# Kernel tuning notes

Measured on AMD Instinct MI355X. Metric: run time of the kernel, lower is better.

## Reference

```python
import jax, jax.numpy as jnp
import numpy as np

B, S, DIM, HEADS, DHEAD = 1, 1992, 2048, 16, 128
NKI_SEQ_ALIGN = 128
EPS = 1e-6


def setup_inputs() -> dict:
    key = jax.random.key(0)
    ks = jax.random.split(key, 8)
    hidden_states = jax.random.normal(ks[0], (B, S, DIM), dtype=jnp.float32)
    # realistic rotary tables, full head_dim with interleaved pair angles
    pos = jnp.arange(S, dtype=jnp.float32)
    inv_freq = 1.0 / (10000.0 ** (jnp.arange(0, DHEAD, 2, dtype=jnp.float32) / DHEAD))
    ang = pos[:, None] * inv_freq[None, :]                      # [S, DHEAD/2]
    full = jnp.stack([ang, ang], axis=-1).reshape(S, DHEAD)     # interleave
    freqs_cos = jnp.cos(full)[None, :, None, :]                 # [1,S,1,DHEAD]
    freqs_sin = jnp.sin(full)[None, :, None, :]
    sc = 0.02
    wq = jax.random.normal(ks[1], (DIM, DIM), dtype=jnp.float32) * sc
    wk = jax.random.normal(ks[2], (DIM, DIM), dtype=jnp.float32) * sc
    wv = jax.random.normal(ks[3], (DIM, DIM), dtype=jnp.float32) * sc
    wo = jax.random.normal(ks[4], (DIM, DIM), dtype=jnp.float32) * sc
    bq = jax.random.normal(ks[5], (DIM,), dtype=jnp.float32) * sc
    bk = jax.random.normal(ks[6], (DIM,), dtype=jnp.float32) * sc
    bv = jax.random.normal(ks[7], (DIM,), dtype=jnp.float32) * sc
    bo = jnp.zeros((DIM,), dtype=jnp.float32)
    norm_q_w = jnp.ones((DIM,), dtype=jnp.float32)
    norm_k_w = jnp.ones((DIM,), dtype=jnp.float32)
    return dict(hidden_states=hidden_states, freqs_cos=freqs_cos, freqs_sin=freqs_sin,
                wq=wq, bq=bq, wk=wk, bk=bk, wv=wv, bv=bv,
                norm_q_w=norm_q_w, norm_k_w=norm_k_w, wo=wo, bo=bo)


def _rms_norm(x, weight, eps=EPS):
    xf = x.astype(jnp.float32)
    var = jnp.mean(xf * xf, axis=-1, keepdims=True)
    return (weight * (xf * jax.lax.rsqrt(var + eps))).astype(x.dtype)


def _apply_rope(x, freqs_cos, freqs_sin):
    # x: [B,H,S,D]; freqs: [1,S,1,D]
    cos = jnp.transpose(freqs_cos[..., 0::2], (0, 2, 1, 3))  # [1,1,S,D/2]
    sin = jnp.transpose(freqs_sin[..., 1::2], (0, 2, 1, 3))
    x1, x2 = x[..., 0::2], x[..., 1::2]
    o1 = x1 * cos - x2 * sin
    o2 = x1 * sin + x2 * cos
    return jnp.stack([o1, o2], axis=-1).reshape(x.shape)


def _attention_padded(q, k, v):
    # Faithful to nki_flash_attention: zero-pad seq to multiple of 128,
    # no masking of padded keys (they contribute logit 0), trim query pad.
    B_, H_, S_, D_ = q.shape
    pad = (-S_) % NKI_SEQ_ALIGN
    if pad:
        pc = [(0, 0), (0, 0), (0, pad), (0, 0)]
        q = jnp.pad(q, pc); k = jnp.pad(k, pc); v = jnp.pad(v, pc)
    scale = 1.0 / np.sqrt(D_)
    scores = jnp.einsum('bhqd,bhkd->bhqk', q, k) * scale
    probs = jax.nn.softmax(scores, axis=-1)
    out = jnp.einsum('bhqk,bhkd->bhqd', probs, v)
    return out[:, :, :S_, :]


def reference(hidden_states, freqs_cos, freqs_sin, wq, bq, wk, bk, wv, bv,
              norm_q_w, norm_k_w, wo, bo):
    b, s, _ = hidden_states.shape
    q = hidden_states @ wq.T + bq
    k = hidden_states @ wk.T + bk
    v = hidden_states @ wv.T + bv
    q = _rms_norm(q, norm_q_w)
    k = _rms_norm(k, norm_k_w)
    hd = q.shape[-1] // HEADS
    q = q.reshape(b, s, HEADS, hd).transpose(0, 2, 1, 3)
    k = k.reshape(b, s, HEADS, hd).transpose(0, 2, 1, 3)
    v = v.reshape(b, s, HEADS, hd).transpose(0, 2, 1, 3)
    q = _apply_rope(q, freqs_cos, freqs_sin)
    k = _apply_rope(k, freqs_cos, freqs_sin)
    o = _attention_padded(q, k, v)
    o = o.transpose(0, 2, 1, 3).reshape(b, s, -1)
    return o @ wo.T + bo
```

## Files before the change

kernel.cpp:

```cpp
#include <hip/hip_runtime.h>
#include <cstdint>

#define S_REAL 1992
#define S_PAD  2048
#define DIMSZ  2048
#define NHEAD  16
#define DHD    128

typedef float f32x4 __attribute__((ext_vector_type(4)));
typedef float f32x16 __attribute__((ext_vector_type(16)));
typedef __bf16 bf16x8 __attribute__((ext_vector_type(8)));
typedef unsigned short u16x8 __attribute__((ext_vector_type(8)));

__device__ __forceinline__ unsigned short f2bf(float f){
  uint32_t u = __float_as_uint(f);
  u += 0x7fffu + ((u >> 16) & 1u);
  return (unsigned short)(u >> 16);
}

__device__ __forceinline__ void gload16(const void* g, void* l){
  __builtin_amdgcn_global_load_lds(
      (const __attribute__((address_space(1))) uint32_t*)g,
      (__attribute__((address_space(3))) uint32_t*)l,
      16, 0, 0);
}

template<int N> __device__ __forceinline__ void waitbar(){
  if constexpr (N == 8)      asm volatile("s_waitcnt vmcnt(8)\n\ts_barrier" ::: "memory");
  else if constexpr (N == 6) asm volatile("s_waitcnt vmcnt(6)\n\ts_barrier" ::: "memory");
  else if constexpr (N == 4) asm volatile("s_waitcnt vmcnt(4)\n\ts_barrier" ::: "memory");
  else if constexpr (N == 3) asm volatile("s_waitcnt vmcnt(3)\n\ts_barrier" ::: "memory");
  else if constexpr (N == 2) asm volatile("s_waitcnt vmcnt(2)\n\ts_barrier" ::: "memory");
  else                       asm volatile("s_waitcnt vmcnt(0)\n\ts_barrier" ::: "memory");
}

__launch_bounds__(256)
__global__ void k_cvt5(const float* __restrict__ s0, const float* __restrict__ s1,
                       const float* __restrict__ s2, const float* __restrict__ s3,
                       const float* __restrict__ s4,
                       unsigned short* __restrict__ d0, unsigned short* __restrict__ d1,
                       unsigned short* __restrict__ d2, unsigned short* __restrict__ d3,
                       unsigned short* __restrict__ d4,
                       int nX, int nW)
{
  int i = blockIdx.x * 256 + threadIdx.x;
  const float* s; unsigned short* d; int j;
  if (i < nX){ s = s0; d = d0; j = i; }
  else {
    int k = i - nX;
    int wsel = k / nW; j = k - wsel * nW;
    s = (wsel == 0) ? s1 : (wsel == 1) ? s2 : (wsel == 2) ? s3 : s4;
    d = (wsel == 0) ? d1 : (wsel == 1) ? d2 : (wsel == 2) ? d3 : d4;
  }
  const float4* sp = (const float4*)s + (size_t)j * 2;
  float4 a = sp[0], b = sp[1];
  u16x8 o;
  o[0]=f2bf(a.x); o[1]=f2bf(a.y); o[2]=f2bf(a.z); o[3]=f2bf(a.w);
  o[4]=f2bf(b.x); o[5]=f2bf(b.y); o[6]=f2bf(b.z); o[7]=f2bf(b.w);
  *((u16x8*)d + j) = o;
}

__launch_bounds__(256, 3)
__global__ void k_g32(const unsigned short* __restrict__ A,
                      const unsigned short* __restrict__ B0,
                      const unsigned short* __restrict__ B1,
                      const unsigned short* __restrict__ B2,
                      const float* __restrict__ bias0,
                      const float* __restrict__ bias1,
                      const float* __restrict__ bias2,
                      float* __restrict__ C0, float* __restrict__ C1, float* __restrict__ C2,
                      int Mreal)
{
  constexpr int BUFE = 8192;
  constexpr int NT   = DIMSZ / 32;
  __shared__ unsigned short lds[3 * BUFE];

  const unsigned short* Bm = (blockIdx.z == 0) ? B0 : ((blockIdx.z == 1) ? B1 : B2);
  const float* bias        = (blockIdx.z == 0) ? bias0 : ((blockIdx.z == 1) ? bias1 : bias2);
  float* C                 = (blockIdx.z == 0) ? C0 : ((blockIdx.z == 1) ? C1 : C2);

  const int fid = blockIdx.x + gridDim.x * blockIdx.y;
  const int q   = (gridDim.x * gridDim.y) >> 3;
  const int nf  = (fid & 7) * q + (fid >> 3);
  const int m0  = (nf >> 4) * 128, n0 = (nf & 15) * 128;

  const int tid = threadIdx.x;
  const int w = tid >> 6, l = tid & 63;
  const int l31 = l & 31, l5 = l >> 5;
  const int wr = (w >> 1) * 64, wc = (w & 1) * 64;

  f32x16 acc[2][2];
  #pragma unroll
  for (int mb = 0; mb < 2; ++mb)
    #pragma unroll
    for (int nb = 0; nb < 2; ++nb)
      #pragma unroll
      for (int r = 0; r < 16; ++r) acc[mb][nb][r] = 0.f;

#define G32_STAGE(TT, BASE) do{                                                   \
    const int k0s = (TT) * 32;                                                    \
    unsigned short* dst = (BASE);                                                 \
    _Pragma("unroll")                                                             \
    for (int i_ = 0; i_ < 2; ++i_){                                               \
      int lin = i_ * 256 + tid;                                                   \
      int r_ = lin >> 2, pos_ = lin & 3;                                          \
      int gr_ = m0 + r_; if (gr_ > Mreal - 1) gr_ = Mreal - 1;                    \
      gload16(A + (size_t)gr_ * DIMSZ + k0s + (pos_ ^ ((r_ >> 1) & 3)) * 8,       \
              dst + lin * 8);                                                     \
    }                                                                             \
    _Pragma("unroll")                                                             \
    for (int i_ = 0; i_ < 2; ++i_){                                               \
      int lin = i_ * 256 + tid;                                                   \
      int r_ = lin >> 2, pos_ = lin & 3;                                          \
      gload16(Bm + (size_t)(n0 + r_) * DIMSZ + k0s + (pos_ ^ ((r_ >> 1) & 3)) * 8,\
              dst + 4096 + lin * 8);                                              \
    }                                                                             \
  } while(0)

#define G32_COMPUTE(BASE) do{                                                     \
    const unsigned short* sb = (BASE);                                            \
    bf16x8 a_[2][2], b_[2][2];                                                    \
    _Pragma("unroll")                                                             \
    for (int mb = 0; mb < 2; ++mb)                                                \
      _Pragma("unroll")                                                           \
      for (int ks = 0; ks < 2; ++ks){                                             \
        int r_ = wr + mb * 32 + l31;                                              \
        int c_ = (ks * 2 + l5) ^ ((r_ >> 1) & 3);                                 \
        a_[mb][ks] = *(const bf16x8*)(sb + r_ * 32 + c_ * 8);                     \
      }                                                                           \
    _Pragma("unroll")                                                             \
    for (int nb = 0; nb < 2; ++nb)                                                \
      _Pragma("unroll")                                                           \
      for (int ks = 0; ks < 2; ++ks){                                             \
        int r_ = wc + nb * 32 + l31;                                              \
        int c_ = (ks * 2 + l5) ^ ((r_ >> 1) & 3);                                 \
        b_[nb][ks] = *(const bf16x8*)(sb + 4096 + r_ * 32 + c_ * 8);              \
      }                                                                           \
    __builtin_amdgcn_s_setprio(1);                                                \
    _Pragma("unroll")                                                             \
    for (int ks = 0; ks < 2; ++ks)                                                \
      _Pragma("unroll")                                                           \
      for (int mb = 0; mb < 2; ++mb)                                              \
        _Pragma("unroll")                                                         \
        for (int nb = 0; nb < 2; ++nb)                                            \
          acc[mb][nb] = __builtin_amdgcn_mfma_f32_32x32x16_bf16(a_[mb][ks],       \
                            b_[nb][ks], acc[mb][nb], 0, 0, 0);                    \
    __builtin_amdgcn_s_setprio(0);                                                \
  } while(0)

  G32_STAGE(0, lds);
  G32_STAGE(1, lds + BUFE);
  int bc = 0, bs = 2;
  for (int tt = 0; tt < NT - 2; ++tt){
    waitbar<4>();
    G32_STAGE(tt + 2, lds + bs * BUFE);
    G32_COMPUTE(lds + bc * BUFE);
    bs = (bs == 2) ? 0 : bs + 1;
    bc = (bc == 2) ? 0 : bc + 1;
  }
  waitbar<4>();
  G32_COMPUTE(lds + bc * BUFE);
  bc = (bc == 2) ? 0 : bc + 1;
  waitbar<0>();
  G32_COMPUTE(lds + bc * BUFE);

#undef G32_STAGE
#undef G32_COMPUTE

  #pragma unroll
  for (int nb = 0; nb < 2; ++nb){
    int col = n0 + wc + nb * 32 + l31;
    float bz = bias[col];
    #pragma unroll
    for (int mb = 0; mb < 2; ++mb){
      #pragma unroll
      for (int r = 0; r < 16; ++r){
        int row = m0 + wr + mb * 32 + (r & 3) + 8 * (r >> 2) + 4 * l5;
        if (row < Mreal) C[(size_t)row * DIMSZ + col] = acc[mb][nb][r] + bz;
      }
    }
  }
}

__launch_bounds__(256)
__global__ void k_normrope2(const float* __restrict__ Qf, const float* __restrict__ Kf,
                            const float* __restrict__ nqw, const float* __restrict__ nkw,
                            const float* __restrict__ fc, const float* __restrict__ fs,
                            unsigned short* __restrict__ OutQ, unsigned short* __restrict__ OutK)
{
  const int s = blockIdx.x;
  const int isK = blockIdx.y;
  const float* Xf = isK ? Kf : Qf;
  const float* nw = isK ? nkw : nqw;
  unsigned short* Out = isK ? OutK : OutQ;
  const float scale = isK ? 1.0f : 0.08838834764831843f;
  const int swz = isK;

  const int t = threadIdx.x;
  const int w = t >> 6, l = t & 63;
  __shared__ float wred[4];
  float v[8];
  float ss = 0.f;
  if (s < S_REAL){
    const float4* p = (const float4*)(Xf + (size_t)s * DIMSZ) + t * 2;
    float4 a = p[0], b = p[1];
    v[0]=a.x; v[1]=a.y; v[2]=a.z; v[3]=a.w; v[4]=b.x; v[5]=b.y; v[6]=b.z; v[7]=b.w;
    #pragma unroll
    for (int j = 0; j < 8; ++j) ss += v[j] * v[j];
  }
  #pragma unroll
  for (int off = 32; off >= 1; off >>= 1) ss += __shfl_xor(ss, off);
  if (l == 0) wred[w] = ss;
  __syncthreads();
  float tot = wred[0] + wred[1] + wred[2] + wred[3];
  float rinv = rsqrtf(tot * (1.f / DIMSZ) + 1e-6f);

  const int h  = t >> 4;
  const int d0 = (t & 15) * 8;
  const int b  = t & 15;
  const int bsw = swz ? (b ^ (s & 7)) : b;
  unsigned short* dst = Out + ((size_t)h * S_PAD + s) * DHD + bsw * 8;
  u16x8 o;
  if (s < S_REAL){
    #pragma unroll
    for (int i = 0; i < 4; ++i){
      float c_ = fc[s * DHD + d0 + 2 * i];
      float s_ = fs[s * DHD + d0 + 2 * i + 1];
      float x1 = v[2 * i]     * rinv * nw[t * 8 + 2 * i];
      float x2 = v[2 * i + 1] * rinv * nw[t * 8 + 2 * i + 1];
      o[2 * i]     = f2bf((x1 * c_ - x2 * s_) * scale);
      o[2 * i + 1] = f2bf((x1 * s_ + x2 * c_) * scale);
    }
  } else {
    #pragma unroll
    for (int j = 0; j < 8; ++j) o[j] = 0;
  }
  *(u16x8*)dst = o;
}

__launch_bounds__(256)
__global__ void k_vtrans(const float* __restrict__ Vf, unsigned short* __restrict__ Vth)
{
  __shared__ unsigned short tile[64][72];
  const int t = threadIdx.x;
  const int s0 = blockIdx.x * 64, c0 = blockIdx.y * 64;
  #pragma unroll
  for (int i = 0; i < 4; ++i){
    int r = (t >> 4) * 4 + i;
    int s = s0 + r;
    int cq = (t & 15) * 4;
    float4 val = {0.f, 0.f, 0.f, 0.f};
    if (s < S_REAL) val = *((const float4*)(Vf + (size_t)s * DIMSZ + c0) + (t & 15));
    tile[r][cq + 0] = f2bf(val.x);
    tile[r][cq + 1] = f2bf(val.y);
    tile[r][cq + 2] = f2bf(val.z);
    tile[r][cq + 3] = f2bf(val.w);
  }
  __syncthreads();
  const int cl = t >> 2;
  const int cc = c0 + cl;
  #pragma unroll
  for (int bi = 0; bi < 2; ++bi){
    int b = (t & 3) * 2 + bi;
    u16x8 o;
    #pragma unroll
    for (int j = 0; j < 8; ++j) o[j] = tile[b * 8 + j][cl];
    int bsw = b ^ (cc & 7);
    *(u16x8*)(Vth + (size_t)cc * S_PAD + s0 + bsw * 8) = o;
  }
}

__launch_bounds__(256)
__global__ void k_attn(const unsigned short* __restrict__ Qh,
                       const unsigned short* __restrict__ Kh,
                       const unsigned short* __restrict__ Vth,
                       unsigned short* __restrict__ O)
{
  __shared__ unsigned short kbuf[2][64 * 128];
  __shared__ unsigned short vbuf[2][128 * 64];
  __shared__ unsigned short pbuf[4][16 * 64];
  const int h = blockIdx.y;
  const int q0 = blockIdx.x * 64;
  const int t = threadIdx.x, w = t >> 6, l = t & 63;
  const int lr = l & 15, lg = l >> 4;

  const unsigned short* Qp = Qh + ((size_t)h * S_PAD + q0 + w * 16 + lr) * DHD;
  bf16x8 qf[4];
  #pragma unroll
  for (int ks = 0; ks < 4; ++ks) qf[ks] = *(const bf16x8*)(Qp + ks * 32 + lg * 8);

  f32x4 acc[8];
  #pragma unroll
  for (int nf = 0; nf < 8; ++nf) acc[nf] = (f32x4){0.f, 0.f, 0.f, 0.f};
  float m = -3.0e38f, lsum = 0.f;

#define ATT_STAGE(KT, BI) do{                                                       \
    _Pragma("unroll")                                                               \
    for (int i_ = 0; i_ < 4; ++i_){                                                 \
      int rK = (w * 4 + i_) * 4 + (l >> 4);                                         \
      gload16(Kh + ((size_t)h * S_PAD + (KT) * 64 + rK) * DHD + (l & 15) * 8,       \
              &kbuf[BI][(w * 4 + i_) * 512]);                                       \
      int rV = (w * 4 + i_) * 8 + (l >> 3);                                         \
      gload16(Vth + ((size_t)h * DHD + rV) * S_PAD + (KT) * 64 + (l & 7) * 8,       \
              &vbuf[BI][(w * 4 + i_) * 512]);                                       \
    }                                                                               \
  } while(0)

  ATT_STAGE(0, 0);
  __syncthreads();

  for (int kt = 0; kt < S_PAD / 64; ++kt){
    const int bi = kt & 1;
    if (kt < S_PAD / 64 - 1) ATT_STAGE(kt + 1, bi ^ 1);

    f32x4 sf[4];
    __builtin_amdgcn_s_setprio(1);
    #pragma unroll
    for (int kvf = 0; kvf < 4; ++kvf){
      sf[kvf] = (f32x4){0.f, 0.f, 0.f, 0.f};
      int r = kvf * 16 + lr;
      #pragma unroll
      for (int ks = 0; ks < 4; ++ks){
        int blk = (ks * 4 + lg) ^ (r & 7);
        bf16x8 kf = *(const bf16x8*)&kbuf[bi][r * 128 + blk * 8];
        sf[kvf] = __builtin_amdgcn_mfma_f32_16x16x32_bf16(kf, qf[ks], sf[kvf], 0, 0, 0);
      }
    }
    __builtin_amdgcn_s_setprio(0);

    float pmax = sf[0][0];
    #pragma unroll
    for (int kvf = 0; kvf < 4; ++kvf)
      #pragma unroll
      for (int j = 0; j < 4; ++j) pmax = fmaxf(pmax, sf[kvf][j]);
    pmax = fmaxf(pmax, __shfl_xor(pmax, 16));
    pmax = fmaxf(pmax, __shfl_xor(pmax, 32));
    float mn = fmaxf(m, pmax);
    float fr = __expf(m - mn);
    m = mn;
    float p[4][4];
    float psum = 0.f;
    #pragma unroll
    for (int kvf = 0; kvf < 4; ++kvf)
      #pragma unroll
      for (int j = 0; j < 4; ++j){ p[kvf][j] = __expf(sf[kvf][j] - mn); psum += p[kvf][j]; }
    lsum = lsum * fr + psum;

    float fv0 = __shfl(fr, lg * 4 + 0);
    float fv1 = __shfl(fr, lg * 4 + 1);
    float fv2 = __shfl(fr, lg * 4 + 2);
    float fv3 = __shfl(fr, lg * 4 + 3);
    f32x4 fv = (f32x4){fv0, fv1, fv2, fv3};
    #pragma unroll
    for (int nf = 0; nf < 8; ++nf) acc[nf] *= fv;

    char* pb = (char*)pbuf[w];
    #pragma unroll
    for (int kvf = 0; kvf < 4; ++kvf){
      uint2 wv;
      wv.x = (uint32_t)f2bf(p[kvf][0]) | ((uint32_t)f2bf(p[kvf][1]) << 16);
      wv.y = (uint32_t)f2bf(p[kvf][2]) | ((uint32_t)f2bf(p[kvf][3]) << 16);
      int byte = lr * 128 + (((kvf * 2 + (lg >> 1)) ^ (lr & 7)) * 16) + (lg & 1) * 8;
      *(uint2*)(pb + byte) = wv;
    }
    bf16x8 pf[2];
    #pragma unroll
    for (int c = 0; c < 2; ++c)
      pf[c] = *(const bf16x8*)(pb + lr * 128 + ((c * 4 + lg) ^ (lr & 7)) * 16);

    __builtin_amdgcn_s_setprio(1);
    #pragma unroll
    for (int nf = 0; nf < 8; ++nf){
      int cc = nf * 16 + lr;
      #pragma unroll
      for (int ks = 0; ks < 2; ++ks){
        int blk = (ks * 4 + lg) ^ (cc & 7);
        bf16x8 vf = *(const bf16x8*)&vbuf[bi][cc * 64 + blk * 8];
        acc[nf] = __builtin_amdgcn_mfma_f32_16x16x32_bf16(pf[ks], vf, acc[nf], 0, 0, 0);
      }
    }
    __builtin_amdgcn_s_setprio(0);

    __syncthreads();
  }
#undef ATT_STAGE

  lsum += __shfl_xor(lsum, 16);
  lsum += __shfl_xor(lsum, 32);
  float ls0 = __shfl(lsum, lg * 4 + 0);
  float ls1 = __shfl(lsum, lg * 4 + 1);
  float ls2 = __shfl(lsum, lg * 4 + 2);
  float ls3 = __shfl(lsum, lg * 4 + 3);
  f32x4 lsv = (f32x4){1.f / ls0, 1.f / ls1, 1.f / ls2, 1.f / ls3};

  #pragma unroll
  for (int nf = 0; nf < 8; ++nf){
    #pragma unroll
    for (int j = 0; j < 4; ++j){
      int row = q0 + w * 16 + lg * 4 + j;
      if (row < S_REAL)
        O[(size_t)row * DIMSZ + h * DHD + nf * 16 + lr] = f2bf(acc[nf][j] * lsv[j]);
    }
  }
}

extern "C" void kernel_launch(void* const* d_in, const int* in_sizes, int n_in,
                              void* d_out, int out_size, void* d_ws, size_t ws_size,
                              hipStream_t stream)
{
  const float* hidden = (const float*)d_in[0];
  const float* fc  = (const float*)d_in[1];
  const float* fs  = (const float*)d_in[2];
  const float* wq  = (const float*)d_in[3];
  const float* bq  = (const float*)d_in[4];
  const float* wk  = (const float*)d_in[5];
  const float* bk  = (const float*)d_in[6];
  const float* wv  = (const float*)d_in[7];
  const float* bv  = (const float*)d_in[8];
  const float* nqw = (const float*)d_in[9];
  const float* nkw = (const float*)d_in[10];
  const float* wo  = (const float*)d_in[11];
  const float* bo  = (const float*)d_in[12];
  float* out = (float*)d_out;

  char* ws = (char*)d_ws;
  size_t off = 0;
  auto alloc = [&](size_t bytes) -> void* {
    void* p = ws + off;
    off += (bytes + 255) & ~(size_t)255;
    return p;
  };
  unsigned short* Xb  = (unsigned short*)alloc((size_t)S_REAL * DIMSZ * 2);
  unsigned short* Wqb = (unsigned short*)alloc((size_t)DIMSZ * DIMSZ * 2);
  unsigned short* Wkb = (unsigned short*)alloc((size_t)DIMSZ * DIMSZ * 2);
  unsigned short* Wvb = (unsigned short*)alloc((size_t)DIMSZ * DIMSZ * 2);
  unsigned short* Wob = (unsigned short*)alloc((size_t)DIMSZ * DIMSZ * 2);
  float* Qf = (float*)alloc((size_t)S_REAL * DIMSZ * 4);
  float* Kf = (float*)alloc((size_t)S_REAL * DIMSZ * 4);
  float* Vf = (float*)alloc((size_t)S_REAL * DIMSZ * 4);
  unsigned short* Qhh = (unsigned short*)alloc((size_t)NHEAD * S_PAD * DHD * 2);
  unsigned short* Khh = (unsigned short*)alloc((size_t)NHEAD * S_PAD * DHD * 2);
  unsigned short* Vth = (unsigned short*)alloc((size_t)NHEAD * DHD * S_PAD * 2);
  unsigned short* Oa  = (unsigned short*)alloc((size_t)S_REAL * DIMSZ * 2);

  {
    int nX = S_REAL * DIMSZ / 8;
    int nW = DIMSZ * DIMSZ / 8;
    int total = nX + 4 * nW;
    k_cvt5<<<total / 256, 256, 0, stream>>>(hidden, wq, wk, wv, wo,
                                            Xb, Wqb, Wkb, Wvb, Wob, nX, nW);
  }

  k_g32<<<dim3(16, 16, 3), 256, 0, stream>>>(Xb, Wqb, Wkb, Wvb, bq, bk, bv,
                                             Qf, Kf, Vf, S_REAL);

  k_normrope2<<<dim3(S_PAD, 2), 256, 0, stream>>>(Qf, Kf, nqw, nkw, fc, fs, Qhh, Khh);

  k_vtrans<<<dim3(S_PAD / 64, DIMSZ / 64), 256, 0, stream>>>(Vf, Vth);

  k_attn<<<dim3(S_PAD / 64, NHEAD), 256, 0, stream>>>(Qhh, Khh, Vth, Oa);

  k_g32<<<dim3(16, 16, 1), 256, 0, stream>>>(Oa, Wob, Wob, Wob, bo, bo, bo,
                                             out, out, out, S_REAL);
}
```

Before: 220.0 us.

## Use 256x256 tile GEMM with 512 threads for QKV projection

Adds a new bf16 MFMA GEMM kernel with 256x256 output tiles, 8 waves per block, a 4-deep LDS ring buffer and a block-index swizzle, and uses it for the fused QKV projection in place of the smaller-tile kernel. Larger tiles raise arithmetic intensity per global load and cut redundant A/B traffic. The split A-fragment loads interleaved with the MFMA phases and the prefetch are meant to overlap memory with compute. The costs are a 192-block grid, fewer than 256 CUs, so some CUs sit idle, plus more registers and 128KB of LDS per block.

```diff
diff --git a/kernel.cpp b/kernel.cpp
--- a/kernel.cpp
+++ b/kernel.cpp
@@ -58,6 +58,135 @@
   o[0]=f2bf(a.x); o[1]=f2bf(a.y); o[2]=f2bf(a.z); o[3]=f2bf(a.w);
   o[4]=f2bf(b.x); o[5]=f2bf(b.y); o[6]=f2bf(b.z); o[7]=f2bf(b.w);
   *((u16x8*)d + j) = o;
+}
+
+__launch_bounds__(512, 2)
+__global__ void k_g256(const unsigned short* __restrict__ A,
+                       const unsigned short* __restrict__ B0,
+                       const unsigned short* __restrict__ B1,
+                       const unsigned short* __restrict__ B2,
+                       const float* __restrict__ bias0,
+                       const float* __restrict__ bias1,
+                       const float* __restrict__ bias2,
+                       float* __restrict__ C0, float* __restrict__ C1, float* __restrict__ C2,
+                       int Mreal)
+{
+  constexpr int BUFE = 16384;
+  constexpr int NT   = DIMSZ / 32;
+  __shared__ unsigned short lds[4 * BUFE];
+
+  const unsigned short* Bm = (blockIdx.z == 0) ? B0 : ((blockIdx.z == 1) ? B1 : B2);
+  const float* bias        = (blockIdx.z == 0) ? bias0 : ((blockIdx.z == 1) ? bias1 : bias2);
+  float* C                 = (blockIdx.z == 0) ? C0 : ((blockIdx.z == 1) ? C1 : C2);
+
+  const int fid = blockIdx.x + (blockIdx.y << 3);
+  const int nf  = (fid & 7) * 8 + (fid >> 3);
+  const int m0  = (nf >> 3) * 256, n0 = (nf & 7) * 256;
+
+  const int tid = threadIdx.x;
+  const int w = tid >> 6, l = tid & 63;
+  const int l31 = l & 31, l5 = l >> 5;
+  const int wrv = (w >> 2) * 128;
+  const int wcv = (w & 3) * 64;
+
+  f32x16 acc[4][2];
+  #pragma unroll
+  for (int mb = 0; mb < 4; ++mb)
+    #pragma unroll
+    for (int nb = 0; nb < 2; ++nb)
+      #pragma unroll
+      for (int r = 0; r < 16; ++r) acc[mb][nb][r] = 0.f;
+
+#define S256(TT, PH) do{                                                          \
+    const int k0s = (TT) * 32;                                                    \
+    unsigned short* dst = &lds[((TT) & 3) * BUFE];                                \
+    int lin = (PH) * 512 + tid;                                                   \
+    int r_ = lin >> 2, cs_ = lin & 3;                                             \
+    int c_ = cs_ ^ (r_ & 3);                                                      \
+    int gr_ = m0 + r_; if (gr_ > Mreal - 1) gr_ = Mreal - 1;                      \
+    gload16(A + (size_t)gr_ * DIMSZ + k0s + c_ * 8, dst + lin * 8);               \
+    gload16(Bm + (size_t)(n0 + r_) * DIMSZ + k0s + c_ * 8, dst + 8192 + lin * 8); \
+  } while(0)
+
+  S256(0, 0); S256(0, 1); S256(1, 0); S256(1, 1); S256(2, 0); S256(2, 1);
+  asm volatile("s_waitcnt vmcnt(8)" ::: "memory");
+  __builtin_amdgcn_s_barrier();
+
+  for (int tt = 0; tt < NT; ++tt){
+    const unsigned short* sb = &lds[(tt & 3) * BUFE];
+    bf16x8 bfr[2][2], af0[2][2];
+
+    #pragma unroll
+    for (int nb = 0; nb < 2; ++nb)
+      #pragma unroll
+      for (int ks = 0; ks < 2; ++ks){
+        int r_ = wcv + nb * 32 + l31;
+        int cs_ = (ks * 2 + l5) ^ (r_ & 3);
+        bfr[nb][ks] = *(const bf16x8*)(sb + 8192 + r_ * 32 + cs_ * 8);
+      }
+    #pragma unroll
+    for (int mb = 0; mb < 2; ++mb)
+      #pragma unroll
+      for (int ks = 0; ks < 2; ++ks){
+        int r_ = wrv + mb * 32 + l31;
+        int cs_ = (ks * 2 + l5) ^ (r_ & 3);
+        af0[mb][ks] = *(const bf16x8*)(sb + r_ * 32 + cs_ * 8);
+      }
+    if (tt < NT - 3) S256(tt + 3, 0);
+    __builtin_amdgcn_s_barrier();
+    __builtin_amdgcn_s_setprio(1);
+    #pragma unroll
+    for (int ks = 0; ks < 2; ++ks)
+      #pragma unroll
+      for (int mb = 0; mb < 2; ++mb)
+        #pragma unroll
+        for (int nb = 0; nb < 2; ++nb)
+          acc[mb][nb] = __builtin_amdgcn_mfma_f32_32x32x16_bf16(af0[mb][ks],
+                            bfr[nb][ks], acc[mb][nb], 0, 0, 0);
+    __builtin_amdgcn_s_setprio(0);
+    __builtin_amdgcn_s_barrier();
+
+    bf16x8 af1[2][2];
+    #pragma unroll
+    for (int mb = 0; mb < 2; ++mb)
+      #pragma unroll
+      for (int ks = 0; ks < 2; ++ks){
+        int r_ = wrv + 64 + mb * 32 + l31;
+        int cs_ = (ks * 2 + l5) ^ (r_ & 3);
+        af1[mb][ks] = *(const bf16x8*)(sb + r_ * 32 + cs_ * 8);
+      }
+    if (tt < NT - 3) S256(tt + 3, 1);
+    __builtin_amdgcn_s_barrier();
+    __builtin_amdgcn_s_setprio(1);
+    #pragma unroll
+    for (int ks = 0; ks < 2; ++ks)
+      #pragma unroll
+      for (int mb = 0; mb < 2; ++mb)
+        #pragma unroll
+        for (int nb = 0; nb < 2; ++nb)
+          acc[2 + mb][nb] = __builtin_amdgcn_mfma_f32_32x32x16_bf16(af1[mb][ks],
+                                bfr[nb][ks], acc[2 + mb][nb], 0, 0, 0);
+    __builtin_amdgcn_s_setprio(0);
+    if (tt < NT - 3)       asm volatile("s_waitcnt vmcnt(8)" ::: "memory");
+    else if (tt == NT - 3) asm volatile("s_waitcnt vmcnt(4)" ::: "memory");
+    else if (tt == NT - 2) asm volatile("s_waitcnt vmcnt(0)" ::: "memory");
+    __builtin_amdgcn_s_barrier();
+  }
+#undef S256
+
+  #pragma unroll
+  for (int nb = 0; nb < 2; ++nb){
+    int col = n0 + wcv + nb * 32 + l31;
+    float bz = bias[col];
+    #pragma unroll
+    for (int mb = 0; mb < 4; ++mb){
+      #pragma unroll
+      for (int r = 0; r < 16; ++r){
+        int row = m0 + wrv + mb * 32 + (r & 3) + 8 * (r >> 2) + 4 * l5;
+        if (row < Mreal) C[(size_t)row * DIMSZ + col] = acc[mb][nb][r] + bz;
+      }
+    }
+  }
 }
 
 __launch_bounds__(256, 3)
@@ -451,8 +580,8 @@
                                             Xb, Wqb, Wkb, Wvb, Wob, nX, nW);
   }
 
-  k_g32<<<dim3(16, 16, 3), 256, 0, stream>>>(Xb, Wqb, Wkb, Wvb, bq, bk, bv,
-                                             Qf, Kf, Vf, S_REAL);
+  k_g256<<<dim3(8, 8, 3), 512, 0, stream>>>(Xb, Wqb, Wkb, Wvb, bq, bk, bv,
+                                            Qf, Kf, Vf, S_REAL);
 
   k_normrope2<<<dim3(S_PAD, 2), 256, 0, stream>>>(Qf, Kf, nqw, nkw, fc, fs, Qhh, Khh);
 
```

Measured after the change: 236.2 us. 7.4% more time.
